# Performance work log

Hardware: AMD Instinct MI355X
Metric: run time of the kernel (lower is better)

## Reference

```python
import jax, jax.numpy as jnp
import numpy as np

H = 2            # attention heads
HID = 128        # hidden_channels
NEG_SLOPE = 0.2  # GATConv leaky_relu slope

N_USER, N_POST, N_ENT = 100000, 50000, 20000
TEXT_D, USER_D, ENT_D = 768, 64, 64
E_PUB, E_REP, E_CON, E_INT, E_FOL = 150000, 300000, 200000, 500000, 500000


def _gat(h_src, h_dst, src, dst, Wsrc, Wdst, asrc, adst, bias):
    """PyG GATConv((-1,-1), C, heads=H, concat=False, add_self_loops=False)."""
    n_dst = h_dst.shape[0]
    C = Wsrc.shape[1] // H
    xs = (h_src @ Wsrc).reshape(-1, H, C)          # [Ns,H,C]
    xd = (h_dst @ Wdst).reshape(-1, H, C)          # [Nd,H,C]
    al_s = jnp.einsum('nhc,hc->nh', xs, asrc)      # [Ns,H]
    al_d = jnp.einsum('nhc,hc->nh', xd, adst)      # [Nd,H]
    e = jax.nn.leaky_relu(al_s[src] + al_d[dst], NEG_SLOPE)   # [E,H]
    m = jax.ops.segment_max(e, dst, num_segments=n_dst)
    m = jnp.where(jnp.isfinite(m), m, 0.0)
    ex = jnp.exp(e - m[dst])
    denom = jax.ops.segment_sum(ex, dst, num_segments=n_dst)
    alpha = ex / (denom[dst] + 1e-16)              # per-dst softmax
    msg = xs[src] * alpha[:, :, None]              # [E,H,C]
    out = jax.ops.segment_sum(msg, dst, num_segments=n_dst)   # [Nd,H,C]
    return out.mean(axis=1) + bias                 # concat=False -> head mean


def setup_inputs() -> dict:
    key = jax.random.key(0)
    ks = jax.random.split(key, 24)
    s = 0.05
    d = {
        'post_cls': jax.random.normal(ks[0], (N_POST, TEXT_D), jnp.float32),
        'user_x': jax.random.normal(ks[1], (N_USER, USER_D), jnp.float32),
        'entity_x': jax.random.normal(ks[2], (N_ENT, ENT_D), jnp.float32),
        'Wpost': jax.random.normal(ks[3], (TEXT_D, HID), jnp.float32) * s,
        'bpost': jnp.zeros((HID,), jnp.float32),
        'Wuser': jax.random.normal(ks[4], (USER_D, HID), jnp.float32) * s,
        'buser': jnp.zeros((HID,), jnp.float32),
        'Went': jax.random.normal(ks[5], (ENT_D, HID), jnp.float32) * s,
        'bent': jnp.zeros((HID,), jnp.float32),
        # 2 layers x 5 relations (publish, repost, contain, interact, follow)
        'gat_Wsrc': jax.random.normal(ks[6], (2, 5, HID, H * HID), jnp.float32) * s,
        'gat_Wdst': jax.random.normal(ks[7], (2, 5, HID, H * HID), jnp.float32) * s,
        'gat_asrc': jax.random.normal(ks[8], (2, 5, H, HID), jnp.float32) * s,
        'gat_adst': jax.random.normal(ks[9], (2, 5, H, HID), jnp.float32) * s,
        'gat_bias': jnp.zeros((2, 5, HID), jnp.float32),
        'Wc1': jax.random.normal(ks[10], (HID, HID // 2), jnp.float32) * s,
        'bc1': jnp.zeros((HID // 2,), jnp.float32),
        'Wc2': jax.random.normal(ks[11], (HID // 2, 1), jnp.float32) * s,
        'bc2': jnp.zeros((1,), jnp.float32),
        'pub_src': jax.random.randint(ks[12], (E_PUB,), 0, N_USER, jnp.int32),
        'pub_dst': jax.random.randint(ks[13], (E_PUB,), 0, N_POST, jnp.int32),
        'rep_src': jax.random.randint(ks[14], (E_REP,), 0, N_USER, jnp.int32),
        'rep_dst': jax.random.randint(ks[15], (E_REP,), 0, N_POST, jnp.int32),
        'con_src': jax.random.randint(ks[16], (E_CON,), 0, N_POST, jnp.int32),
        'con_dst': jax.random.randint(ks[17], (E_CON,), 0, N_ENT, jnp.int32),
        'int_src': jax.random.randint(ks[18], (E_INT,), 0, N_USER, jnp.int32),
        'int_dst': jax.random.randint(ks[19], (E_INT,), 0, N_USER, jnp.int32),
        'fol_src': jax.random.randint(ks[20], (E_FOL,), 0, N_USER, jnp.int32),
        'fol_dst': jax.random.randint(ks[21], (E_FOL,), 0, N_USER, jnp.int32),
    }
    return d


def _forward(post_cls, user_x, entity_x, Wpost, bpost, Wuser, buser, Went, bent,
             gat_Wsrc, gat_Wdst, gat_asrc, gat_adst, gat_bias,
             Wc1, bc1, Wc2, bc2, edges):
    h = {
        'post': post_cls @ Wpost + bpost,
        'user': user_x @ Wuser + buser,
        'entity': entity_x @ Went + bent,
    }
    for l in range(2):
        def g(r, h_src, h_dst, src, dst):
            return _gat(h_src, h_dst, src, dst,
                        gat_Wsrc[l, r], gat_Wdst[l, r],
                        gat_asrc[l, r], gat_adst[l, r], gat_bias[l, r])
        # HeteroConv aggr='sum' over edge types sharing a dst node type
        new_post = (g(0, h['user'], h['post'], edges['pub_src'], edges['pub_dst'])
                    + g(1, h['user'], h['post'], edges['rep_src'], edges['rep_dst']))
        new_ent = g(2, h['post'], h['entity'], edges['con_src'], edges['con_dst'])
        new_user = (g(3, h['user'], h['user'], edges['int_src'], edges['int_dst'])
                    + g(4, h['user'], h['user'], edges['fol_src'], edges['fol_dst']))
        h = {'post': jax.nn.relu(new_post),
             'user': jax.nn.relu(new_user),
             'entity': jax.nn.relu(new_ent)}
    # classifier (dropout inactive at inference)
    z = jax.nn.relu(h['post'] @ Wc1 + bc1)
    out = z @ Wc2 + bc2
    return out.squeeze(-1)   # [n_posts]


def reference(post_cls, user_x, entity_x, Wpost, bpost, Wuser, buser, Went, bent,
              gat_Wsrc, gat_Wdst, gat_asrc, gat_adst, gat_bias,
              Wc1, bc1, Wc2, bc2,
              pub_src, pub_dst, rep_src, rep_dst, con_src, con_dst,
              int_src, int_dst, fol_src, fol_dst):
    edges = dict(pub_src=pub_src, pub_dst=pub_dst, rep_src=rep_src, rep_dst=rep_dst,
                 con_src=con_src, con_dst=con_dst, int_src=int_src, int_dst=int_dst,
                 fol_src=fol_src, fol_dst=fol_dst)
    return _forward(post_cls, user_x, entity_x, Wpost, bpost, Wuser, buser, Went, bent,
                    gat_Wsrc, gat_Wdst, gat_asrc, gat_adst, gat_bias,
                    Wc1, bc1, Wc2, bc2, edges)
```

## Files before the change

### kernel.cpp

```cpp
#include <hip/hip_runtime.h>
#include <cstdint>
#include <cstddef>

#define N_USER 100000
#define N_POST 50000
#define TEXT_D 768
#define USER_D 64
#define E_TOT 1450000
#define N_TOT 300000

typedef unsigned short ushort_t;
typedef float f4v __attribute__((ext_vector_type(4)));
typedef short s8v __attribute__((ext_vector_type(8)));
typedef unsigned short u4v __attribute__((ext_vector_type(4)));
typedef unsigned short u8v __attribute__((ext_vector_type(8)));

__device__ __forceinline__ float leaky(float v) { return v > 0.f ? v : 0.2f * v; }
__device__ __forceinline__ void split_bf(float x, ushort_t& hi, ushort_t& lo) {
  unsigned u = __float_as_uint(x);
  hi = (ushort_t)(u >> 16);
  float r = x - __uint_as_float(u & 0xFFFF0000u);
  lo = (ushort_t)(__float_as_uint(r) >> 16);
}

struct Ptrs4 { const int* p[4]; };

__global__ void wvec_kernel(const float* __restrict__ W, const float* __restrict__ av,
                            float* __restrict__ wv) {
  int b = blockIdx.x;
  int lr = b / 2, h = b % 2;
  const float* Wp = W + ((size_t)lr * 128 * 256) + (size_t)threadIdx.x * 256 + h * 128;
  const float* ap = av + (size_t)(lr * 2 + h) * 128;
  float acc = 0.f;
  for (int c = 0; c < 128; ++c) acc += Wp[c] * ap[c];
  wv[(size_t)(lr * 2 + h) * 128 + threadIdx.x] = acc;
}

__global__ void wt_prep(const float* __restrict__ W, ushort_t* __restrict__ WTh,
                        ushort_t* __restrict__ WTl, int K, int C) {
  int k = blockIdx.x * 256 + threadIdx.x;
  int c = blockIdx.y;
  if (k >= K) return;
  ushort_t h, l;
  split_bf(W[(size_t)k * C + c], h, l);
  WTh[(size_t)c * K + k] = h;
  WTl[(size_t)c * K + k] = l;
}

__global__ void stk_prep(const float* __restrict__ Wa, const float* __restrict__ Wb,
                         ushort_t* __restrict__ STh, ushort_t* __restrict__ STl) {
  int rel = blockIdx.x;
  int c = blockIdx.y;
  int t = threadIdx.x;
  const float* W = rel ? Wb : Wa;
  float v = W[(size_t)(t & 127) * 256 + (size_t)(t >> 7) * 128 + c];
  ushort_t hh, ll;
  split_bf(v, hh, ll);
  size_t idx = (size_t)c * 512 + (size_t)rel * 256 + t;
  STh[idx] = hh;
  STl[idx] = ll;
}

__global__ void bias_sum(const float* __restrict__ gbias, float* __restrict__ BS) {
  int c = threadIdx.x;
  BS[c]       = gbias[0 * 640 + 0 * 128 + c] + gbias[0 * 640 + 1 * 128 + c];
  BS[128 + c] = gbias[0 * 640 + 3 * 128 + c] + gbias[0 * 640 + 4 * 128 + c];
  BS[256 + c] = gbias[1 * 640 + 0 * 128 + c] + gbias[1 * 640 + 1 * 128 + c];
}

template <int CF, bool BIAS>
__global__ __launch_bounds__(256) void gemm_mfma(const float* __restrict__ X,
                                                 const ushort_t* __restrict__ WTh,
                                                 const ushort_t* __restrict__ WTl,
                                                 const float* __restrict__ bv,
                                                 float* __restrict__ Out,
                                                 int N, int K) {
  __shared__ ushort_t Ah[64][40], Al[64][40];
  __shared__ ushort_t Bh[CF * 16][40], Bl[CF * 16][40];
  int t = threadIdx.x;
  int L = t & 63;
  int wv = t >> 6;
  int m = L & 15, quad = L >> 4;
  int row0 = blockIdx.x * 64;

  f4v acc[CF];
#pragma unroll
  for (int cf = 0; cf < CF; ++cf) acc[cf] = (f4v){0.f, 0.f, 0.f, 0.f};

  int nk = K >> 5;
  for (int kb = 0; kb < nk; ++kb) {
    int k0 = kb * 32;
#pragma unroll
    for (int i = 0; i < 2; ++i) {
      int s = t + 256 * i;
      int r = s >> 3, k4 = s & 7;
      int row = row0 + r;
      float4 v = make_float4(0.f, 0.f, 0.f, 0.f);
      if (row < N) v = *(const float4*)(X + (size_t)row * K + k0 + k4 * 4);
      ushort_t hx, lx, hy, ly, hz, lz, hw, lw;
      split_bf(v.x, hx, lx); split_bf(v.y, hy, ly);
      split_bf(v.z, hz, lz); split_bf(v.w, hw, lw);
      u4v h, l;
      h[0] = hx; h[1] = hy; h[2] = hz; h[3] = hw;
      l[0] = lx; l[1] = ly; l[2] = lz; l[3] = lw;
      *(u4v*)&Ah[r][k4 * 4] = h;
      *(u4v*)&Al[r][k4 * 4] = l;
    }
#pragma unroll
    for (int i = 0; i < CF / 4; ++i) {
      int s = t + 256 * i;
      int c = s >> 2, ch = s & 3;
      *(u8v*)&Bh[c][ch * 8] = *(const u8v*)(WTh + (size_t)c * K + k0 + ch * 8);
      *(u8v*)&Bl[c][ch * 8] = *(const u8v*)(WTl + (size_t)c * K + k0 + ch * 8);
    }
    __syncthreads();
    s8v a_h = *(const s8v*)&Ah[wv * 16 + m][quad * 8];
    s8v a_l = *(const s8v*)&Al[wv * 16 + m][quad * 8];
#pragma unroll
    for (int cf = 0; cf < CF; ++cf) {
      s8v b_h = *(const s8v*)&Bh[cf * 16 + m][quad * 8];
      s8v b_l = *(const s8v*)&Bl[cf * 16 + m][quad * 8];
      acc[cf] = __builtin_amdgcn_mfma_f32_16x16x32_bf16(a_h, b_h, acc[cf], 0, 0, 0);
      acc[cf] = __builtin_amdgcn_mfma_f32_16x16x32_bf16(a_h, b_l, acc[cf], 0, 0, 0);
      acc[cf] = __builtin_amdgcn_mfma_f32_16x16x32_bf16(a_l, b_h, acc[cf], 0, 0, 0);
    }
    __syncthreads();
  }

  float bvs[CF];
#pragma unroll
  for (int cf = 0; cf < CF; ++cf) bvs[cf] = BIAS ? bv[cf * 16 + m] : 0.f;
#pragma unroll
  for (int j = 0; j < 4; ++j) {
    int row = row0 + wv * 16 + quad * 4 + j;
    if (row < N) {
      float* o = Out + (size_t)row * (CF * 16) + m;
#pragma unroll
      for (int cf = 0; cf < CF; ++cf) o[cf * 16] = acc[cf][j] + bvs[cf];
    }
  }
}

template <int NK>
__global__ __launch_bounds__(256) void gemm_split(const ushort_t* __restrict__ Agh,
                                                  const ushort_t* __restrict__ Agl,
                                                  const ushort_t* __restrict__ Bgh,
                                                  const ushort_t* __restrict__ Bgl,
                                                  const float* __restrict__ bv,
                                                  float* __restrict__ Out, int N) {
  constexpr int K = NK * 64;
  __shared__ __align__(16) ushort_t LAh[64 * 64], LAl[64 * 64];
  __shared__ __align__(16) ushort_t LBh[128 * 64], LBl[128 * 64];
  int t = threadIdx.x;
  int lane = t & 63, w = t >> 6;
  int m = lane & 15, quad = lane >> 4;
  int wr = w >> 1, wc = w & 1;
  int row0 = blockIdx.x * 64;

  int arow[2], acol[2];
#pragma unroll
  for (int i = 0; i < 2; ++i) {
    int p = t + 256 * i;
    int r = p >> 3, q = (p & 7) ^ (r & 7);
    int row = row0 + r;
    if (row >= N) row = N - 1;
    arow[i] = row; acol[i] = q * 8;
  }
  int bcol[4], bq[4];
#pragma unroll
  for (int i = 0; i < 4; ++i) {
    int p = t + 256 * i;
    int c = p >> 3, q = (p & 7) ^ (c & 7);
    bcol[i] = c; bq[i] = q * 8;
  }

  f4v acc[2][4];
#pragma unroll
  for (int mt = 0; mt < 2; ++mt)
#pragma unroll
    for (int ct = 0; ct < 4; ++ct) acc[mt][ct] = (f4v){0.f, 0.f, 0.f, 0.f};

  u8v rah[2], ral[2], rbh[4], rbl[4];
  auto LOAD = [&](int kb) {
    int k0 = kb * 64;
#pragma unroll
    for (int i = 0; i < 2; ++i) {
      rah[i] = *(const u8v*)(Agh + (size_t)arow[i] * K + k0 + acol[i]);
      ral[i] = *(const u8v*)(Agl + (size_t)arow[i] * K + k0 + acol[i]);
    }
#pragma unroll
    for (int i = 0; i < 4; ++i) {
      rbh[i] = *(const u8v*)(Bgh + (size_t)bcol[i] * K + k0 + bq[i]);
      rbl[i] = *(const u8v*)(Bgl + (size_t)bcol[i] * K + k0 + bq[i]);
    }
  };
  LOAD(0);
  for (int kb = 0; kb < NK; ++kb) {
    __syncthreads();
#pragma unroll
    for (int i = 0; i < 2; ++i) {
      *(u8v*)&LAh[(size_t)(t + 256 * i) * 8] = rah[i];
      *(u8v*)&LAl[(size_t)(t + 256 * i) * 8] = ral[i];
    }
#pragma unroll
    for (int i = 0; i < 4; ++i) {
      *(u8v*)&LBh[(size_t)(t + 256 * i) * 8] = rbh[i];
      *(u8v*)&LBl[(size_t)(t + 256 * i) * 8] = rbl[i];
    }
    __syncthreads();
    if (kb + 1 < NK) LOAD(kb + 1);
#pragma unroll
    for (int ks = 0; ks < 2; ++ks) {
      s8v ah[2], alo[2], bh[4], blo[4];
#pragma unroll
      for (int mt = 0; mt < 2; ++mt) {
        int r = wr * 32 + mt * 16 + m;
        int gr = r * 8 + ((ks * 4 + quad) ^ (m & 7));
        ah[mt] = *(const s8v*)&LAh[(size_t)gr * 8];
        alo[mt] = *(const s8v*)&LAl[(size_t)gr * 8];
      }
#pragma unroll
      for (int ct = 0; ct < 4; ++ct) {
        int c = wc * 64 + ct * 16 + m;
        int gc = c * 8 + ((ks * 4 + quad) ^ (m & 7));
        bh[ct] = *(const s8v*)&LBh[(size_t)gc * 8];
        blo[ct] = *(const s8v*)&LBl[(size_t)gc * 8];
      }
#pragma unroll
      for (int mt = 0; mt < 2; ++mt)
#pragma unroll
        for (int ct = 0; ct < 4; ++ct) {
          acc[mt][ct] = __builtin_amdgcn_mfma_f32_16x16x32_bf16(ah[mt], bh[ct], acc[mt][ct], 0, 0, 0);
          acc[mt][ct] = __builtin_amdgcn_mfma_f32_16x16x32_bf16(ah[mt], blo[ct], acc[mt][ct], 0, 0, 0);
          acc[mt][ct] = __builtin_amdgcn_mfma_f32_16x16x32_bf16(alo[mt], bh[ct], acc[mt][ct], 0, 0, 0);
        }
    }
  }
  float bb[4];
#pragma unroll
  for (int ct = 0; ct < 4; ++ct) bb[ct] = bv[wc * 64 + ct * 16 + m];
#pragma unroll
  for (int mt = 0; mt < 2; ++mt)
#pragma unroll
    for (int j = 0; j < 4; ++j) {
      int row = row0 + wr * 32 + mt * 16 + quad * 4 + j;
      if (row < N) {
        float* o = Out + (size_t)row * 128 + wc * 64 + m;
#pragma unroll
        for (int ct = 0; ct < 4; ++ct) o[ct * 16] = fmaxf(acc[mt][ct][j] + bb[ct], 0.f);
      }
    }
}

__device__ __forceinline__ void rel_of(int g, int& r, int& loc, int& nb) {
  if (g < 450000) {
    if (g < 150000) { r = 0; loc = g;          nb = 0; }
    else            { r = 1; loc = g - 150000; nb = 50000; }
  } else if (g < 950000)  { r = 2; loc = g - 450000;  nb = 100000; }
  else                    { r = 3; loc = g - 950000;  nb = 200000; }
}
__global__ void histc_kernel(Ptrs4 dsts, int* __restrict__ cnt) {
  int g = blockIdx.x * 256 + threadIdx.x;
  if (g >= E_TOT) return;
  int r, loc, nb;
  rel_of(g, r, loc, nb);
  atomicAdd(&cnt[nb + dsts.p[r][loc]], 1);
}
__global__ __launch_bounds__(256) void scan1_kernel(const int* __restrict__ cnt,
                                                    int* __restrict__ excl,
                                                    int* __restrict__ partials, int Nd) {
  __shared__ int sb[256];
  int t = threadIdx.x;
  int base = blockIdx.x * 1024 + t * 4;
  int v[4];
#pragma unroll
  for (int j = 0; j < 4; ++j) v[j] = (base + j < Nd) ? cnt[base + j] : 0;
  int tot = v[0] + v[1] + v[2] + v[3];
  sb[t] = tot;
  __syncthreads();
  for (int off = 1; off < 256; off <<= 1) {
    int x = 0;
    if (t >= off) x = sb[t - off];
    __syncthreads();
    sb[t] += x;
    __syncthreads();
  }
  int ex = sb[t] - tot;
  if (t == 255) partials[blockIdx.x] = sb[t];
  int run = ex;
#pragma unroll
  for (int j = 0; j < 4; ++j) {
    if (base + j < Nd) excl[base + j] = run;
    run += v[j];
  }
}
__global__ __launch_bounds__(512) void scan2_kernel(int* __restrict__ partials, int B) {
  __shared__ int sb[512];
  int t = threadIdx.x;
  int v = (t < B) ? partials[t] : 0;
  sb[t] = v;
  __syncthreads();
  for (int off = 1; off < 512; off <<= 1) {
    int x = 0;
    if (t >= off) x = sb[t - off];
    __syncthreads();
    sb[t] += x;
    __syncthreads();
  }
  if (t < B) partials[t] = sb[t] - v;
}
__global__ void scan3_kernel(const int* __restrict__ excl, const int* __restrict__ partials,
                             int* __restrict__ rowptr, int* __restrict__ cursor) {
  int i = blockIdx.x * 256 + threadIdx.x;
  if (i < N_TOT) {
    int v = excl[i] + partials[i >> 10];
    rowptr[i] = v;
    cursor[i] = v;
  }
  if (i == 0) rowptr[N_TOT] = E_TOT;
}
__global__ void scatterc_kernel(Ptrs4 srcs, Ptrs4 dsts,
                                int* __restrict__ cursor, int* __restrict__ csrc) {
  int g = blockIdx.x * 256 + threadIdx.x;
  if (g >= E_TOT) return;
  int r, loc, nb;
  rel_of(g, r, loc, nb);
  int p = atomicAdd(&cursor[nb + dsts.p[r][loc]], 1);
  csrc[p] = srcs.p[r][loc];
}

__global__ __launch_bounds__(256) void logits2_kernel(const float* __restrict__ H,
                                                      const float* __restrict__ wsA,
                                                      const float* __restrict__ wsB,
                                                      float* __restrict__ alsA,
                                                      float* __restrict__ alsB, int Ns) {
  int n = blockIdx.x * 4 + (threadIdx.x >> 6);
  int lane = threadIdx.x & 63;
  if (n >= Ns) return;
  const float* hr = H + (size_t)n * 128;
  float ha = hr[lane], hb = hr[lane + 64];
  float p0 = ha * wsA[lane] + hb * wsA[lane + 64];
  float p1 = ha * wsA[128 + lane] + hb * wsA[192 + lane];
  float p2 = ha * wsB[lane] + hb * wsB[lane + 64];
  float p3 = ha * wsB[128 + lane] + hb * wsB[192 + lane];
#pragma unroll
  for (int mk = 32; mk; mk >>= 1) {
    p0 += __shfl_xor(p0, mk); p1 += __shfl_xor(p1, mk);
    p2 += __shfl_xor(p2, mk); p3 += __shfl_xor(p3, mk);
  }
  if (lane == 0) {
    *(float2*)(alsA + 2 * (size_t)n) = make_float2(p0, p1);
    *(float2*)(alsB + 2 * (size_t)n) = make_float2(p2, p3);
  }
}

__device__ __forceinline__ void dst_tvals(const float* __restrict__ Hd, const float* __restrict__ wdv,
                                          int d, int lane, float& t0, float& t1) {
  const float* hr = Hd + (size_t)d * 128;
  float ha = hr[lane], hb = hr[lane + 64];
  t0 = ha * wdv[lane] + hb * wdv[lane + 64];
  t1 = ha * wdv[128 + lane] + hb * wdv[192 + lane];
#pragma unroll
  for (int mk = 32; mk; mk >>= 1) { t0 += __shfl_xor(t0, mk); t1 += __shfl_xor(t1, mk); }
}

__device__ __forceinline__ void aggG_rel(const int* __restrict__ rowptr,
                                         const int* __restrict__ csrc,
                                         const float* __restrict__ als,
                                         const float* __restrict__ Hs,
                                         float t0, float t1, int d, int h, int s,
                                         int lane, ushort_t* __restrict__ GrowH,
                                         ushort_t* __restrict__ GrowL) {
  int start = rowptr[d], end = rowptr[d + 1];
  float den0 = 0.f, den1 = 0.f;
  float a0[4] = {0.f, 0.f, 0.f, 0.f}, a1[4] = {0.f, 0.f, 0.f, 0.f};
  if (end > start) {
    int last = end - 1;
    for (int b0 = start; b0 < end; b0 += 8) {
      int e[4]; bool vl[4]; int sid[4];
#pragma unroll
      for (int j = 0; j < 4; ++j) {
        int ee = b0 + 2 * j + h;
        vl[j] = ee < end;
        e[j] = vl[j] ? ee : last;
      }
#pragma unroll
      for (int j = 0; j < 4; ++j) sid[j] = csrc[e[j]];
      float2 al[4]; f4v x[4];
#pragma unroll
      for (int j = 0; j < 4; ++j) {
        al[j] = *(const float2*)(als + 2 * (size_t)sid[j]);
        x[j] = *(const f4v*)(Hs + (size_t)sid[j] * 128 + 4 * s);
      }
#pragma unroll
      for (int j = 0; j < 4; ++j) {
        float w0 = vl[j] ? __expf(leaky(al[j].x + t0)) : 0.f;
        float w1 = vl[j] ? __expf(leaky(al[j].y + t1)) : 0.f;
        den0 += w0; den1 += w1;
#pragma unroll
        for (int q = 0; q < 4; ++q) {
          a0[q] += w0 * x[j][q];
          a1[q] += w1 * x[j][q];
        }
      }
    }
  }
  den0 += __shfl_xor(den0, 32);
  den1 += __shfl_xor(den1, 32);
  float i0 = 0.5f / (den0 + 1e-16f);
  float i1 = 0.5f / (den1 + 1e-16f);
  f4v o0, o1;
#pragma unroll
  for (int q = 0; q < 4; ++q) {
    float u = a0[q] + __shfl_xor(a0[q], 32);
    float v = a1[q] + __shfl_xor(a1[q], 32);
    o0[q] = u * i0;
    o1[q] = v * i1;
  }
  if (lane < 32) {
    u4v g0h, g0l, g1h, g1l;
#pragma unroll
    for (int q = 0; q < 4; ++q) {
      ushort_t hh, ll;
      split_bf(o0[q], hh, ll); g0h[q] = hh; g0l[q] = ll;
      split_bf(o1[q], hh, ll); g1h[q] = hh; g1l[q] = ll;
    }
    *(u4v*)(GrowH + 4 * s) = g0h;
    *(u4v*)(GrowL + 4 * s) = g0l;
    *(u4v*)(GrowH + 128 + 4 * s) = g1h;
    *(u4v*)(GrowL + 128 + 4 * s) = g1l;
  }
}

__global__ __launch_bounds__(256) void aggG2_kernel(const int* __restrict__ rowA,
                                                    const int* __restrict__ rowB,
                                                    const int* __restrict__ csrc,
                                                    const float* __restrict__ alsA,
                                                    const float* __restrict__ alsB,
                                                    const float* __restrict__ wdvA,
                                                    const float* __restrict__ wdvB,
                                                    const float* __restrict__ Hs,
                                                    const float* __restrict__ Hd,
                                                    ushort_t* __restrict__ Gh,
                                                    ushort_t* __restrict__ Gl,
                                                    int Nd, int dOff) {
  int w = threadIdx.x >> 6;
  int lane = threadIdx.x & 63;
  int dl = blockIdx.x * 2 + (w >> 1);
  int rel = w & 1;
  if (dl >= Nd) return;
  int d = dl + dOff;
  const int* rp = rel ? rowB : rowA;
  const float* alsP = rel ? alsB : alsA;
  const float* wdv = rel ? wdvB : wdvA;
  float t0, t1;
  dst_tvals(Hd, wdv, d, lane, t0, t1);
  int h = lane >> 5, s = lane & 31;
  aggG_rel(rp, csrc, alsP, Hs, t0, t1, d, h, s, lane,
           Gh + (size_t)dl * 512 + rel * 256, Gl + (size_t)dl * 512 + rel * 256);
}

__global__ __launch_bounds__(256) void classifier_kernel(const float* __restrict__ Hp,
                                                         const float* __restrict__ Wc1, const float* __restrict__ bc1,
                                                         const float* __restrict__ Wc2, const float* __restrict__ bc2,
                                                         float* __restrict__ out, int N) {
  __shared__ float sW[128 * 64];
  int t = threadIdx.x;
#pragma unroll
  for (int i = 0; i < 8; ++i) ((float4*)sW)[t + 256 * i] = ((const float4*)Wc1)[t + 256 * i];
  __syncthreads();
  int lane = t & 63, wv = t >> 6;
  float b = bc1[lane], w2 = Wc2[lane], b2 = bc2[0];
#pragma unroll
  for (int nn = 0; nn < 2; ++nn) {
    int n = blockIdx.x * 8 + wv * 2 + nn;
    if (n >= N) continue;
    const float* hr = Hp + (size_t)n * 128;
    float accz = b;
    for (int k = 0; k < 128; ++k) accz += hr[k] * sW[k * 64 + lane];
    float z = fmaxf(accz, 0.f) * w2;
#pragma unroll
    for (int off = 32; off; off >>= 1) z += __shfl_down(z, off);
    if (lane == 0) out[n] = z + b2;
  }
}

extern "C" void kernel_launch(void* const* d_in, const int* in_sizes, int n_in,
                              void* d_out, int out_size, void* d_ws, size_t ws_size,
                              hipStream_t stream) {
  const float* post_cls = (const float*)d_in[0];
  const float* user_x   = (const float*)d_in[1];
  const float* Wpost = (const float*)d_in[3];
  const float* bpost = (const float*)d_in[4];
  const float* Wuser = (const float*)d_in[5];
  const float* buser = (const float*)d_in[6];
  const float* gWsrc = (const float*)d_in[9];
  const float* gWdst = (const float*)d_in[10];
  const float* gasrc = (const float*)d_in[11];
  const float* gadst = (const float*)d_in[12];
  const float* gbias = (const float*)d_in[13];
  const float* Wc1 = (const float*)d_in[14];
  const float* bc1 = (const float*)d_in[15];
  const float* Wc2 = (const float*)d_in[16];
  const float* bc2 = (const float*)d_in[17];
  Ptrs4 SRCS, DSTS;
  SRCS.p[0] = (const int*)d_in[18]; DSTS.p[0] = (const int*)d_in[19];
  SRCS.p[1] = (const int*)d_in[20]; DSTS.p[1] = (const int*)d_in[21];
  SRCS.p[2] = (const int*)d_in[24]; DSTS.p[2] = (const int*)d_in[25];
  SRCS.p[3] = (const int*)d_in[26]; DSTS.p[3] = (const int*)d_in[27];
  float* out = (float*)d_out;
  (void)ws_size; (void)in_sizes; (void)n_in; (void)out_size;

  float* Wf = (float*)d_ws;
  size_t o = 0;
  float* WDSTV = Wf + o; o += 2560;
  float* WSRCV = Wf + o; o += 2560;
  float* BS    = Wf + o; o += 384;
  float* ALSa  = Wf + o; o += (size_t)N_USER * 2;
  float* ALSb  = Wf + o; o += (size_t)N_USER * 2;
  float* HU    = Wf + o; o += (size_t)N_USER * 128;
  float* HP    = Wf + o; o += (size_t)N_POST * 128;
  float* TMP   = Wf + o; o += (size_t)N_POST * 128;
  int* Wi = (int*)(Wf + o);
  size_t io = 0;
  int* RP   = Wi + io; io += N_TOT + 1;
  int* CURS = Wi + io; io += N_TOT;
  int* CNT  = Wi + io; io += N_TOT;
  int* EXCL = Wi + io; io += N_TOT;
  int* PART = Wi + io; io += 512;
  int* CSRC = Wi + io; io += E_TOT;
  io = (io + 7) & ~(size_t)7;
  ushort_t* Wu = (ushort_t*)(Wi + io);
  size_t uo = 0;
  ushort_t* PWh = Wu + uo; uo += 128 * TEXT_D;
  ushort_t* PWl = Wu + uo; uo += 128 * TEXT_D;
  ushort_t* UWh = Wu + uo; uo += 128 * USER_D;
  ushort_t* UWl = Wu + uo; uo += 128 * USER_D;
  ushort_t* STh[3]; ushort_t* STl[3];
  for (int i = 0; i < 3; ++i) {
    STh[i] = Wu + uo; uo += 128 * 512;
    STl[i] = Wu + uo; uo += 128 * 512;
  }
  ushort_t* Gh = Wu + uo; uo += (size_t)N_POST * 512;
  ushort_t* Gl = Wu + uo; uo += (size_t)N_POST * 512;

  const int NOFF_PUB = 0, NOFF_REP = 50000, NOFF_INT = 100000, NOFF_FOL = 200000;

  (void)hipMemsetAsync(CNT, 0, (size_t)N_TOT * sizeof(int), stream);
  histc_kernel<<<(E_TOT + 255) / 256, 256, 0, stream>>>(DSTS, CNT);
  int B = (N_TOT + 1023) / 1024;
  scan1_kernel<<<B, 256, 0, stream>>>(CNT, EXCL, PART, N_TOT);
  scan2_kernel<<<1, 512, 0, stream>>>(PART, B);
  scan3_kernel<<<(N_TOT + 255) / 256, 256, 0, stream>>>(EXCL, PART, RP, CURS);
  scatterc_kernel<<<(E_TOT + 255) / 256, 256, 0, stream>>>(SRCS, DSTS, CURS, CSRC);

  wt_prep<<<dim3(3, 128), 256, 0, stream>>>(Wpost, PWh, PWl, TEXT_D, 128);
  wt_prep<<<dim3(1, 128), 256, 0, stream>>>(Wuser, UWh, UWl, USER_D, 128);
  stk_prep<<<dim3(2, 128), 256, 0, stream>>>(gWsrc + (size_t)0 * 32768, gWsrc + (size_t)1 * 32768, STh[0], STl[0]);
  stk_prep<<<dim3(2, 128), 256, 0, stream>>>(gWsrc + (size_t)3 * 32768, gWsrc + (size_t)4 * 32768, STh[1], STl[1]);
  stk_prep<<<dim3(2, 128), 256, 0, stream>>>(gWsrc + (size_t)5 * 32768, gWsrc + (size_t)6 * 32768, STh[2], STl[2]);
  wvec_kernel<<<20, 128, 0, stream>>>(gWdst, gadst, WDSTV);
  wvec_kernel<<<20, 128, 0, stream>>>(gWsrc, gasrc, WSRCV);
  bias_sum<<<1, 128, 0, stream>>>(gbias, BS);

  gemm_mfma<8, true><<<(N_POST + 63) / 64, 256, 0, stream>>>(
      post_cls, PWh, PWl, bpost, HP, N_POST, TEXT_D);
  gemm_mfma<8, true><<<(N_USER + 63) / 64, 256, 0, stream>>>(
      user_x, UWh, UWl, buser, HU, N_USER, USER_D);

  logits2_kernel<<<(N_USER + 3) / 4, 256, 0, stream>>>(
      HU, WSRCV + 0 * 256, WSRCV + 1 * 256, ALSa, ALSb, N_USER);
  aggG2_kernel<<<(N_POST + 1) / 2, 256, 0, stream>>>(
      RP + NOFF_PUB, RP + NOFF_REP, CSRC, ALSa, ALSb,
      WDSTV + 0 * 256, WDSTV + 1 * 256, HU, HP, Gh, Gl, N_POST, 0);
  gemm_split<8><<<(N_POST + 63) / 64, 256, 0, stream>>>(
      Gh, Gl, STh[0], STl[0], BS + 0, HP, N_POST);

  logits2_kernel<<<(N_USER + 3) / 4, 256, 0, stream>>>(
      HU, WSRCV + 3 * 256, WSRCV + 4 * 256, ALSa, ALSb, N_USER);
  aggG2_kernel<<<(50000 + 1) / 2, 256, 0, stream>>>(
      RP + NOFF_INT, RP + NOFF_FOL, CSRC, ALSa, ALSb,
      WDSTV + 3 * 256, WDSTV + 4 * 256, HU, HU, Gh, Gl, 50000, 0);
  gemm_split<8><<<(50000 + 63) / 64, 256, 0, stream>>>(
      Gh, Gl, STh[1], STl[1], BS + 128, TMP, 50000);
  aggG2_kernel<<<(50000 + 1) / 2, 256, 0, stream>>>(
      RP + NOFF_INT, RP + NOFF_FOL, CSRC, ALSa, ALSb,
      WDSTV + 3 * 256, WDSTV + 4 * 256, HU, HU, Gh, Gl, 50000, 50000);
  gemm_split<8><<<(50000 + 63) / 64, 256, 0, stream>>>(
      Gh, Gl, STh[1], STl[1], BS + 128, HU + (size_t)50000 * 128, 50000);
  (void)hipMemcpyAsync(HU, TMP, (size_t)50000 * 128 * sizeof(float),
                       hipMemcpyDeviceToDevice, stream);

  logits2_kernel<<<(N_USER + 3) / 4, 256, 0, stream>>>(
      HU, WSRCV + 5 * 256, WSRCV + 6 * 256, ALSa, ALSb, N_USER);
  aggG2_kernel<<<(N_POST + 1) / 2, 256, 0, stream>>>(
      RP + NOFF_PUB, RP + NOFF_REP, CSRC, ALSa, ALSb,
      WDSTV + 5 * 256, WDSTV + 6 * 256, HU, HP, Gh, Gl, N_POST, 0);
  gemm_split<8><<<(N_POST + 63) / 64, 256, 0, stream>>>(
      Gh, Gl, STh[2], STl[2], BS + 256, HP, N_POST);

  classifier_kernel<<<(N_POST + 7) / 8, 256, 0, stream>>>(HP, Wc1, bc1, Wc2, bc2, out, N_POST);
}
```

Measured before the change: 1.067 ms.

## Two-pass bucketed CSR scatter and register-prefetch GEMM tiles

The CSR build now scatters edges first into coarse buckets of 64 destination nodes, then runs a second per-bucket pass that scatters into final slots, so the random writes land in a small, cache-local region. This targets the scattered atomics and writes over the whole 1.45M-edge array, at the cost of an extra pass and two extra edge-sized buffers. Separately, the MFMA GEMM loads the next K tile's global data into registers while the current tile is computed, overlapping global load latency with math at the cost of more registers.

New measurement: 1.251 ms. 1.17x slower.

```diff
diff --git a/kernel.cpp b/kernel.cpp
--- a/kernel.cpp
+++ b/kernel.cpp
@@ -8,6 +8,7 @@
 #define USER_D 64
 #define E_TOT 1450000
 #define N_TOT 300000
+#define NBUK 4688
 
 typedef unsigned short ushort_t;
 typedef float f4v __attribute__((ext_vector_type(4)));
@@ -87,19 +88,35 @@
 #pragma unroll
   for (int cf = 0; cf < CF; ++cf) acc[cf] = (f4v){0.f, 0.f, 0.f, 0.f};
 
-  int nk = K >> 5;
-  for (int kb = 0; kb < nk; ++kb) {
+  float4 pa[2];
+  u8v pbh[CF / 4], pbl[CF / 4];
+
+  auto LOADR = [&](int kb) {
     int k0 = kb * 32;
 #pragma unroll
     for (int i = 0; i < 2; ++i) {
       int s = t + 256 * i;
       int r = s >> 3, k4 = s & 7;
       int row = row0 + r;
-      float4 v = make_float4(0.f, 0.f, 0.f, 0.f);
-      if (row < N) v = *(const float4*)(X + (size_t)row * K + k0 + k4 * 4);
+      pa[i] = make_float4(0.f, 0.f, 0.f, 0.f);
+      if (row < N) pa[i] = *(const float4*)(X + (size_t)row * K + k0 + k4 * 4);
+    }
+#pragma unroll
+    for (int i = 0; i < CF / 4; ++i) {
+      int s = t + 256 * i;
+      int c = s >> 2, ch = s & 3;
+      pbh[i] = *(const u8v*)(WTh + (size_t)c * K + k0 + ch * 8);
+      pbl[i] = *(const u8v*)(WTl + (size_t)c * K + k0 + ch * 8);
+    }
+  };
+  auto WRITER = [&]() {
+#pragma unroll
+    for (int i = 0; i < 2; ++i) {
+      int s = t + 256 * i;
+      int r = s >> 3, k4 = s & 7;
       ushort_t hx, lx, hy, ly, hz, lz, hw, lw;
-      split_bf(v.x, hx, lx); split_bf(v.y, hy, ly);
-      split_bf(v.z, hz, lz); split_bf(v.w, hw, lw);
+      split_bf(pa[i].x, hx, lx); split_bf(pa[i].y, hy, ly);
+      split_bf(pa[i].z, hz, lz); split_bf(pa[i].w, hw, lw);
       u4v h, l;
       h[0] = hx; h[1] = hy; h[2] = hz; h[3] = hw;
       l[0] = lx; l[1] = ly; l[2] = lz; l[3] = lw;
@@ -110,10 +127,17 @@
     for (int i = 0; i < CF / 4; ++i) {
       int s = t + 256 * i;
       int c = s >> 2, ch = s & 3;
-      *(u8v*)&Bh[c][ch * 8] = *(const u8v*)(WTh + (size_t)c * K + k0 + ch * 8);
-      *(u8v*)&Bl[c][ch * 8] = *(const u8v*)(WTl + (size_t)c * K + k0 + ch * 8);
-    }
-    __syncthreads();
+      *(u8v*)&Bh[c][ch * 8] = pbh[i];
+      *(u8v*)&Bl[c][ch * 8] = pbl[i];
+    }
+  };
+
+  int nk = K >> 5;
+  LOADR(0);
+  for (int kb = 0; kb < nk; ++kb) {
+    WRITER();
+    __syncthreads();
+    if (kb + 1 < nk) LOADR(kb + 1);
     s8v a_h = *(const s8v*)&Ah[wv * 16 + m][quad * 8];
     s8v a_l = *(const s8v*)&Al[wv * 16 + m][quad * 8];
 #pragma unroll
@@ -319,14 +343,37 @@
   }
   if (i == 0) rowptr[N_TOT] = E_TOT;
 }
-__global__ void scatterc_kernel(Ptrs4 srcs, Ptrs4 dsts,
-                                int* __restrict__ cursor, int* __restrict__ csrc) {
+
+__global__ void binit_kernel(const int* __restrict__ rowptr, int* __restrict__ bcur) {
+  int b = blockIdx.x * 256 + threadIdx.x;
+  if (b < NBUK) bcur[b] = rowptr[b << 6];
+}
+__global__ void binA_kernel(Ptrs4 srcs, Ptrs4 dsts, int* __restrict__ bcur,
+                            int* __restrict__ edid, int* __restrict__ esrc) {
   int g = blockIdx.x * 256 + threadIdx.x;
   if (g >= E_TOT) return;
   int r, loc, nb;
   rel_of(g, r, loc, nb);
-  int p = atomicAdd(&cursor[nb + dsts.p[r][loc]], 1);
-  csrc[p] = srcs.p[r][loc];
+  int did = nb + dsts.p[r][loc];
+  int p = atomicAdd(&bcur[did >> 6], 1);
+  edid[p] = did;
+  esrc[p] = srcs.p[r][loc];
+}
+__global__ __launch_bounds__(256) void scatterf_kernel(const int* __restrict__ rowptr,
+                                                       const int* __restrict__ edid,
+                                                       const int* __restrict__ esrc,
+                                                       int* __restrict__ cursor,
+                                                       int* __restrict__ csrc) {
+  int b = blockIdx.x;
+  int lo = rowptr[b << 6];
+  int hiIdx = (b + 1) << 6;
+  if (hiIdx > N_TOT) hiIdx = N_TOT;
+  int hi = rowptr[hiIdx];
+  for (int e = lo + (int)threadIdx.x; e < hi; e += 256) {
+    int did = edid[e];
+    int p = atomicAdd(&cursor[did], 1);
+    csrc[p] = esrc[e];
+  }
 }
 
 __global__ __launch_bounds__(256) void logits2_kernel(const float* __restrict__ H,
@@ -529,6 +576,9 @@
   int* EXCL = Wi + io; io += N_TOT;
   int* PART = Wi + io; io += 512;
   int* CSRC = Wi + io; io += E_TOT;
+  int* BCUR = Wi + io; io += 4704;
+  int* EDID = Wi + io; io += E_TOT;
+  int* ESRC = Wi + io; io += E_TOT;
   io = (io + 7) & ~(size_t)7;
   ushort_t* Wu = (ushort_t*)(Wi + io);
   size_t uo = 0;
@@ -552,7 +602,9 @@
   scan1_kernel<<<B, 256, 0, stream>>>(CNT, EXCL, PART, N_TOT);
   scan2_kernel<<<1, 512, 0, stream>>>(PART, B);
   scan3_kernel<<<(N_TOT + 255) / 256, 256, 0, stream>>>(EXCL, PART, RP, CURS);
-  scatterc_kernel<<<(E_TOT + 255) / 256, 256, 0, stream>>>(SRCS, DSTS, CURS, CSRC);
+  binit_kernel<<<(NBUK + 255) / 256, 256, 0, stream>>>(RP, BCUR);
+  binA_kernel<<<(E_TOT + 255) / 256, 256, 0, stream>>>(SRCS, DSTS, BCUR, EDID, ESRC);
+  scatterf_kernel<<<NBUK, 256, 0, stream>>>(RP, EDID, ESRC, CURS, CSRC);
 
   wt_prep<<<dim3(3, 128), 256, 0, stream>>>(Wpost, PWh, PWl, TEXT_D, 128);
   wt_prep<<<dim3(1, 128), 256, 0, stream>>>(Wuser, UWh, UWl, USER_D, 128);
```
